# Optimization experiments

Measured on AMD Instinct MI355X. Metric: run time of the kernel, lower is better.

The kernel has to match this reference:

```python
import jax, jax.numpy as jnp
import numpy as np

V, E, H, L = 50257, 1024, 1024, 512


def setup_inputs() -> dict:
    key = jax.random.key(0)
    ks = jax.random.split(key, 12)
    s = 0.02
    return {
        'input': jax.random.randint(ks[0], (1,), 0, V),
        'hidden': jax.random.normal(ks[1], (1, 1, H), dtype=jnp.float32),
        'encoder_outputs': jax.random.normal(ks[2], (L, H), dtype=jnp.float32),
        'emb_table': jax.random.normal(ks[3], (V, E), dtype=jnp.float32) * s,
        'attn_W': jax.random.normal(ks[4], (L, E + H), dtype=jnp.float32) * s,
        'attn_b': jax.random.normal(ks[5], (L,), dtype=jnp.float32) * s,
        'W_ih': jax.random.normal(ks[6], (3 * H, E + H), dtype=jnp.float32) * s,
        'W_hh': jax.random.normal(ks[7], (3 * H, H), dtype=jnp.float32) * s,
        'b_ih': jax.random.normal(ks[8], (3 * H,), dtype=jnp.float32) * s,
        'b_hh': jax.random.normal(ks[9], (3 * H,), dtype=jnp.float32) * s,
        'out_W': jax.random.normal(ks[10], (V, H), dtype=jnp.float32) * s,
        'out_b': jax.random.normal(ks[11], (V,), dtype=jnp.float32) * s,
    }


def reference(input, hidden, encoder_outputs, emb_table, attn_W, attn_b,
              W_ih, W_hh, b_ih, b_hh, out_W, out_b):
    # Dropout is inference-identity here.
    embedded = emb_table[input].reshape(1, E)                      # [1, E]
    h = hidden[0]                                                  # [1, H]
    attn_in = jnp.concatenate([embedded, h], axis=1)               # [1, E+H]
    attn_weights = jax.nn.softmax(attn_in @ attn_W.T + attn_b, axis=1)  # [1, L]
    attn_applied = attn_weights @ encoder_outputs                  # [1, H]
    x = jnp.concatenate([embedded, attn_applied], axis=1)          # [1, E+H]
    # PyTorch GRU cell, gate order (r, z, n)
    gi = x @ W_ih.T + b_ih                                         # [1, 3H]
    gh = h @ W_hh.T + b_hh                                         # [1, 3H]
    i_r, i_z, i_n = gi[:, :H], gi[:, H:2 * H], gi[:, 2 * H:]
    h_r, h_z, h_n = gh[:, :H], gh[:, H:2 * H], gh[:, 2 * H:]
    r = jax.nn.sigmoid(i_r + h_r)
    z = jax.nn.sigmoid(i_z + h_z)
    n = jnp.tanh(i_n + r * h_n)
    h_new = (1.0 - z) * n + z * h                                  # [1, H]
    log_probs = jax.nn.log_softmax(h_new @ out_W.T + out_b, axis=1)  # [1, V]
    return log_probs, h_new[None], attn_weights
```

## Files before the change

### kernel.cpp

```cpp
#include <hip/hip_runtime.h>
#include <math.h>

#define V 50257
#define E 1024
#define H 1024
#define L 512

#define OUT_H  50257
#define OUT_AW 51281

#define WS_S    0
#define WS_X    1024
#define WS_GH   3072
#define WS_GI   6144
#define WS_BM   10240
#define WS_BS   12288

__device__ __forceinline__ float dot4(const float4 a, const float4 b) {
    return a.x * b.x + a.y * b.y + a.z * b.z + a.w * b.w;
}

__device__ __forceinline__ float wave_sum(float v) {
    for (int off = 32; off > 0; off >>= 1) v += __shfl_down(v, off, 64);
    return v;
}

__global__ void k1_scores_gh(const int* __restrict__ input,
                             const float* __restrict__ hidden,
                             const float* __restrict__ emb_table,
                             const float* __restrict__ attn_W,
                             const float* __restrict__ attn_b,
                             const float* __restrict__ W_hh,
                             const float* __restrict__ b_hh,
                             float* __restrict__ ws) {
    const int t = threadIdx.x;
    const int lane = t & 63;
    const int gwave = blockIdx.x * 4 + (t >> 6);
    const float4* h4 = (const float4*)hidden;
    const float* embrow = emb_table + (size_t)input[0] * E;

    if (gwave < L) {
        const float4* emb4 = (const float4*)embrow;
        const float4* w4 = (const float4*)(attn_W + (size_t)gwave * (E + H));
        float acc = 0.f;
#pragma unroll
        for (int k = 0; k < 8; ++k) {
            int i = lane + 64 * k;
            float4 a = (k < 4) ? emb4[i] : h4[i - E / 4];
            acc += dot4(a, w4[i]);
        }
        acc = wave_sum(acc);
        if (lane == 0) ws[WS_S + gwave] = acc + attn_b[gwave];
    } else if (gwave < L + 3 * H) {
        int k = gwave - L;
        const float4* w4 = (const float4*)(W_hh + (size_t)k * H);
        float acc = 0.f;
#pragma unroll
        for (int ii = 0; ii < 4; ++ii) {
            int i = lane + 64 * ii;
            acc += dot4(h4[i], w4[i]);
        }
        acc = wave_sum(acc);
        if (lane == 0) ws[WS_GH + k] = acc + b_hh[k];
    } else if (gwave < 3600) {
        ws[WS_X + E + (gwave - 3584) * 64 + lane] = 0.f;
    } else if (gwave < 3616) {
        int i = (gwave - 3600) * 64 + lane;
        ws[WS_X + i] = embrow[i];
    }
}

__global__ void k2_softmax_applied(const float* __restrict__ enc,
                                   float* __restrict__ ws,
                                   float* __restrict__ out) {
    __shared__ float w[512];
    __shared__ float redm[4], reds[4];
    __shared__ float bmax, bsum;
    const int t = threadIdx.x;
    const int lane = t & 63, wid = t >> 6;

    float v0 = ws[WS_S + t];
    float v1 = ws[WS_S + 256 + t];
    float m = fmaxf(v0, v1);
    for (int off = 32; off > 0; off >>= 1) m = fmaxf(m, __shfl_down(m, off, 64));
    if (lane == 0) redm[wid] = m;
    __syncthreads();
    if (t == 0) bmax = fmaxf(fmaxf(redm[0], redm[1]), fmaxf(redm[2], redm[3]));
    __syncthreads();
    float e0 = expf(v0 - bmax), e1 = expf(v1 - bmax);
    float s = wave_sum(e0 + e1);
    if (lane == 0) reds[wid] = s;
    __syncthreads();
    if (t == 0) bsum = reds[0] + reds[1] + reds[2] + reds[3];
    __syncthreads();
    float inv = 1.f / bsum;
    w[t] = e0 * inv;
    w[256 + t] = e1 * inv;
    if (blockIdx.x == 0) {
        out[OUT_AW + t] = e0 * inv;
        out[OUT_AW + 256 + t] = e1 * inv;
    }
    __syncthreads();

    const int j = (blockIdx.x & 3) * 256 + t;
    const int l0 = (blockIdx.x >> 2) * 64;
    float acc = 0.f;
#pragma unroll 8
    for (int l = l0; l < l0 + 64; ++l)
        acc += w[l] * enc[(size_t)l * H + j];
    atomicAdd(&ws[WS_X + E + j], acc);
}

__global__ void k3_gi(const float* __restrict__ W_ih, const float* __restrict__ b_ih,
                      float* __restrict__ ws) {
    const int lane = threadIdx.x & 63;
    const int gwave = blockIdx.x * 4 + (threadIdx.x >> 6);
    const float4* x4 = (const float4*)(ws + WS_X);
    const float4* w4 = (const float4*)(W_ih + (size_t)gwave * (E + H));
    float acc = 0.f;
#pragma unroll
    for (int k = 0; k < 8; ++k) {
        int i = lane + 64 * k;
        acc += dot4(x4[i], w4[i]);
    }
    acc = wave_sum(acc);
    if (lane == 0) ws[WS_GI + gwave] = acc + b_ih[gwave];
}

__global__ void k4_logits(const float* __restrict__ hidden,
                          const float* __restrict__ out_W,
                          const float* __restrict__ out_b,
                          float* __restrict__ ws,
                          float* __restrict__ out) {
    __shared__ float hn[H];
    __shared__ float wm[4], wsum[4];
    const int t = threadIdx.x;
    const int lane = t & 63, wid = t >> 6;

#pragma unroll
    for (int c = 0; c < 4; ++c) {
        int k = t + 256 * c;
        float gir = ws[WS_GI + k],         ghr = ws[WS_GH + k];
        float giz = ws[WS_GI + H + k],     ghz = ws[WS_GH + H + k];
        float gin = ws[WS_GI + 2 * H + k], ghn = ws[WS_GH + 2 * H + k];
        float r = 1.f / (1.f + expf(-(gir + ghr)));
        float z = 1.f / (1.f + expf(-(giz + ghz)));
        float n = tanhf(gin + r * ghn);
        float v = (1.f - z) * n + z * hidden[k];
        hn[k] = v;
        if (blockIdx.x == 0) out[OUT_H + k] = v;
    }
    __syncthreads();

    const float4* hn4 = (const float4*)hn;
    const int gwave = blockIdx.x * 4 + wid;
    float m = -INFINITY, s = 0.f;
    for (int row = gwave; row < V; row += 8192) {
        const float4* w4 = (const float4*)(out_W + (size_t)row * H);
        float acc = 0.f;
#pragma unroll
        for (int ii = 0; ii < 4; ++ii) {
            int i = lane + 64 * ii;
            acc += dot4(hn4[i], w4[i]);
        }
        acc = wave_sum(acc);
        if (lane == 0) {
            float lg = acc + out_b[row];
            out[row] = lg;
            if (lg > m) { s = s * expf(m - lg) + 1.f; m = lg; }
            else        { s += expf(lg - m); }
        }
    }
    if (lane == 0) { wm[wid] = m; wsum[wid] = s; }
    __syncthreads();
    if (t == 0) {
        float M = fmaxf(fmaxf(wm[0], wm[1]), fmaxf(wm[2], wm[3]));
        float S = wsum[0] * expf(wm[0] - M) + wsum[1] * expf(wm[1] - M)
                + wsum[2] * expf(wm[2] - M) + wsum[3] * expf(wm[3] - M);
        ws[WS_BM + blockIdx.x] = M;
        ws[WS_BS + blockIdx.x] = S;
    }
}

__global__ void k5_logprobs(const float* __restrict__ ws, float* __restrict__ out) {
    __shared__ float redm[4], reds[4];
    __shared__ float off_s;
    const int t = threadIdx.x;
    const int lane = t & 63, wid = t >> 6;
    float m = -INFINITY, s = 0.f;
#pragma unroll
    for (int c = 0; c < 8; ++c) {
        int b = t + 256 * c;
        float bm = ws[WS_BM + b], bs = ws[WS_BS + b];
        float M2 = fmaxf(m, bm);
        s = s * expf(m - M2) + bs * expf(bm - M2);
        m = M2;
    }
    for (int off = 32; off > 0; off >>= 1) {
        float mo = __shfl_down(m, off, 64);
        float so = __shfl_down(s, off, 64);
        float M2 = fmaxf(m, mo);
        s = s * expf(m - M2) + so * expf(mo - M2);
        m = M2;
    }
    if (lane == 0) { redm[wid] = m; reds[wid] = s; }
    __syncthreads();
    if (t == 0) {
        float M = redm[0], S = reds[0];
        for (int i = 1; i < 4; ++i) {
            float M2 = fmaxf(M, redm[i]);
            S = S * expf(M - M2) + reds[i] * expf(redm[i] - M2);
            M = M2;
        }
        off_s = M + logf(S);
    }
    __syncthreads();
    int i = blockIdx.x * 256 + t;
    if (i < V) out[i] -= off_s;
}

extern "C" void kernel_launch(void* const* d_in, const int* in_sizes, int n_in,
                              void* d_out, int out_size, void* d_ws, size_t ws_size,
                              hipStream_t stream) {
    const int*   input   = (const int*)d_in[0];
    const float* hidden  = (const float*)d_in[1];
    const float* enc     = (const float*)d_in[2];
    const float* emb     = (const float*)d_in[3];
    const float* attn_W  = (const float*)d_in[4];
    const float* attn_b  = (const float*)d_in[5];
    const float* W_ih    = (const float*)d_in[6];
    const float* W_hh    = (const float*)d_in[7];
    const float* b_ih    = (const float*)d_in[8];
    const float* b_hh    = (const float*)d_in[9];
    const float* out_W   = (const float*)d_in[10];
    const float* out_b   = (const float*)d_in[11];
    float* out = (float*)d_out;
    float* ws  = (float*)d_ws;

    k1_scores_gh<<<904, 256, 0, stream>>>(input, hidden, emb, attn_W, attn_b, W_hh, b_hh, ws);
    k2_softmax_applied<<<32, 256, 0, stream>>>(enc, ws, out);
    k3_gi<<<768, 256, 0, stream>>>(W_ih, b_ih, ws);
    k4_logits<<<2048, 256, 0, stream>>>(hidden, out_W, out_b, ws, out);
    k5_logprobs<<<197, 256, 0, stream>>>(ws, out);
}
```

Measured before the change: 443.2 us.

## Fuse all stages into one persistent kernel with grid barriers and out_W prefetch

Replaces the five kernel launches with one persistent kernel of 1024 blocks that syncs stages through atomic grid barriers in workspace. While 768 blocks run the attention/GRU-input stages, the other 256 blocks stream out_W rows to warm the cache before the logits stage. The aim is to remove launch gaps and overlap loading the large output matrix with the dependent front stages. It depends on all blocks being co-resident, since the spin barriers would deadlock otherwise (a guard counter bounds the wait), and it adds barrier latency and a memset.

```diff
diff --git a/kernel.cpp b/kernel.cpp
--- a/kernel.cpp
+++ b/kernel.cpp
@@ -14,7 +14,11 @@
 #define WS_GH   3072
 #define WS_GI   6144
 #define WS_BM   10240
-#define WS_BS   12288
+#define WS_BS   11264
+#define WS_BAR  12288
+
+#define NB 1024
+#define NC 768
 
 __device__ __forceinline__ float dot4(const float4 a, const float4 b) {
     return a.x * b.x + a.y * b.y + a.z * b.z + a.w * b.w;
@@ -25,117 +29,153 @@
     return v;
 }
 
-__global__ void k1_scores_gh(const int* __restrict__ input,
-                             const float* __restrict__ hidden,
-                             const float* __restrict__ emb_table,
-                             const float* __restrict__ attn_W,
-                             const float* __restrict__ attn_b,
-                             const float* __restrict__ W_hh,
-                             const float* __restrict__ b_hh,
-                             float* __restrict__ ws) {
+__device__ __forceinline__ void gbar(int* bar, int idx, int target) {
+    __syncthreads();
+    if (threadIdx.x == 0) {
+        __threadfence();
+        __hip_atomic_fetch_add(&bar[idx], 1, __ATOMIC_RELEASE, __HIP_MEMORY_SCOPE_AGENT);
+        int guard = 0;
+        while (__hip_atomic_load(&bar[idx], __ATOMIC_ACQUIRE, __HIP_MEMORY_SCOPE_AGENT) < target) {
+            __builtin_amdgcn_s_sleep(2);
+            if (++guard > (1 << 22)) break;
+        }
+    }
+    __syncthreads();
+    __threadfence();
+}
+
+__global__ __launch_bounds__(256, 4)
+void fused(const int* __restrict__ input,
+           const float* __restrict__ hidden,
+           const float* __restrict__ enc,
+           const float* __restrict__ emb_table,
+           const float* __restrict__ attn_W,
+           const float* __restrict__ attn_b,
+           const float* __restrict__ W_ih,
+           const float* __restrict__ W_hh,
+           const float* __restrict__ b_ih,
+           const float* __restrict__ b_hh,
+           const float* __restrict__ out_W,
+           const float* __restrict__ out_b,
+           float* __restrict__ out,
+           float* __restrict__ ws) {
+    __shared__ float w[512];
+    __shared__ float hn[H];
+    __shared__ float redm[4], reds[4];
+    __shared__ float bmax, bsum, off_s;
+
     const int t = threadIdx.x;
     const int lane = t & 63;
-    const int gwave = blockIdx.x * 4 + (t >> 6);
+    const int wid = t >> 6;
+    const int bid = blockIdx.x;
+    int* bar = (int*)(ws + WS_BAR);
     const float4* h4 = (const float4*)hidden;
-    const float* embrow = emb_table + (size_t)input[0] * E;
-
-    if (gwave < L) {
-        const float4* emb4 = (const float4*)embrow;
-        const float4* w4 = (const float4*)(attn_W + (size_t)gwave * (E + H));
-        float acc = 0.f;
-#pragma unroll
-        for (int k = 0; k < 8; ++k) {
-            int i = lane + 64 * k;
-            float4 a = (k < 4) ? emb4[i] : h4[i - E / 4];
-            acc += dot4(a, w4[i]);
-        }
-        acc = wave_sum(acc);
-        if (lane == 0) ws[WS_S + gwave] = acc + attn_b[gwave];
-    } else if (gwave < L + 3 * H) {
-        int k = gwave - L;
-        const float4* w4 = (const float4*)(W_hh + (size_t)k * H);
-        float acc = 0.f;
-#pragma unroll
-        for (int ii = 0; ii < 4; ++ii) {
-            int i = lane + 64 * ii;
-            acc += dot4(h4[i], w4[i]);
-        }
-        acc = wave_sum(acc);
-        if (lane == 0) ws[WS_GH + k] = acc + b_hh[k];
-    } else if (gwave < 3600) {
-        ws[WS_X + E + (gwave - 3584) * 64 + lane] = 0.f;
-    } else if (gwave < 3616) {
-        int i = (gwave - 3600) * 64 + lane;
-        ws[WS_X + i] = embrow[i];
-    }
-}
-
-__global__ void k2_softmax_applied(const float* __restrict__ enc,
-                                   float* __restrict__ ws,
-                                   float* __restrict__ out) {
-    __shared__ float w[512];
-    __shared__ float redm[4], reds[4];
-    __shared__ float bmax, bsum;
-    const int t = threadIdx.x;
-    const int lane = t & 63, wid = t >> 6;
-
-    float v0 = ws[WS_S + t];
-    float v1 = ws[WS_S + 256 + t];
-    float m = fmaxf(v0, v1);
-    for (int off = 32; off > 0; off >>= 1) m = fmaxf(m, __shfl_down(m, off, 64));
-    if (lane == 0) redm[wid] = m;
-    __syncthreads();
-    if (t == 0) bmax = fmaxf(fmaxf(redm[0], redm[1]), fmaxf(redm[2], redm[3]));
-    __syncthreads();
-    float e0 = expf(v0 - bmax), e1 = expf(v1 - bmax);
-    float s = wave_sum(e0 + e1);
-    if (lane == 0) reds[wid] = s;
-    __syncthreads();
-    if (t == 0) bsum = reds[0] + reds[1] + reds[2] + reds[3];
-    __syncthreads();
-    float inv = 1.f / bsum;
-    w[t] = e0 * inv;
-    w[256 + t] = e1 * inv;
-    if (blockIdx.x == 0) {
-        out[OUT_AW + t] = e0 * inv;
-        out[OUT_AW + 256 + t] = e1 * inv;
-    }
-    __syncthreads();
-
-    const int j = (blockIdx.x & 3) * 256 + t;
-    const int l0 = (blockIdx.x >> 2) * 64;
-    float acc = 0.f;
-#pragma unroll 8
-    for (int l = l0; l < l0 + 64; ++l)
-        acc += w[l] * enc[(size_t)l * H + j];
-    atomicAdd(&ws[WS_X + E + j], acc);
-}
-
-__global__ void k3_gi(const float* __restrict__ W_ih, const float* __restrict__ b_ih,
-                      float* __restrict__ ws) {
-    const int lane = threadIdx.x & 63;
-    const int gwave = blockIdx.x * 4 + (threadIdx.x >> 6);
-    const float4* x4 = (const float4*)(ws + WS_X);
-    const float4* w4 = (const float4*)(W_ih + (size_t)gwave * (E + H));
-    float acc = 0.f;
-#pragma unroll
-    for (int k = 0; k < 8; ++k) {
-        int i = lane + 64 * k;
-        acc += dot4(x4[i], w4[i]);
-    }
-    acc = wave_sum(acc);
-    if (lane == 0) ws[WS_GI + gwave] = acc + b_ih[gwave];
-}
-
-__global__ void k4_logits(const float* __restrict__ hidden,
-                          const float* __restrict__ out_W,
-                          const float* __restrict__ out_b,
-                          float* __restrict__ ws,
-                          float* __restrict__ out) {
-    __shared__ float hn[H];
-    __shared__ float wm[4], wsum[4];
-    const int t = threadIdx.x;
-    const int lane = t & 63, wid = t >> 6;
+
+    if (bid < NC) {
+        const float* embrow = emb_table + (size_t)input[0] * E;
+
+        for (int gw = bid * 4 + wid; gw < 3616; gw += NC * 4) {
+            if (gw < L) {
+                const float4* emb4 = (const float4*)embrow;
+                const float4* w4 = (const float4*)(attn_W + (size_t)gw * (E + H));
+                float acc = 0.f;
+#pragma unroll
+                for (int k = 0; k < 8; ++k) {
+                    int i = lane + 64 * k;
+                    float4 a = (k < 4) ? emb4[i] : h4[i - E / 4];
+                    acc += dot4(a, w4[i]);
+                }
+                acc = wave_sum(acc);
+                if (lane == 0) ws[WS_S + gw] = acc + attn_b[gw];
+            } else if (gw < L + 3 * H) {
+                int k = gw - L;
+                const float4* w4 = (const float4*)(W_hh + (size_t)k * H);
+                float acc = 0.f;
+#pragma unroll
+                for (int ii = 0; ii < 4; ++ii) {
+                    int i = lane + 64 * ii;
+                    acc += dot4(h4[i], w4[i]);
+                }
+                acc = wave_sum(acc);
+                if (lane == 0) ws[WS_GH + k] = acc + b_hh[k];
+            } else if (gw < 3600) {
+                ws[WS_X + E + (gw - 3584) * 64 + lane] = 0.f;
+            } else {
+                int i = (gw - 3600) * 64 + lane;
+                ws[WS_X + i] = embrow[i];
+            }
+        }
+
+        gbar(bar, 0, NC);
+
+        if (bid < 128) {
+            float v0 = ws[WS_S + t];
+            float v1 = ws[WS_S + 256 + t];
+            float m = fmaxf(v0, v1);
+            for (int off = 32; off > 0; off >>= 1) m = fmaxf(m, __shfl_down(m, off, 64));
+            if (lane == 0) redm[wid] = m;
+            __syncthreads();
+            if (t == 0) bmax = fmaxf(fmaxf(redm[0], redm[1]), fmaxf(redm[2], redm[3]));
+            __syncthreads();
+            float e0 = expf(v0 - bmax), e1 = expf(v1 - bmax);
+            float s = wave_sum(e0 + e1);
+            if (lane == 0) reds[wid] = s;
+            __syncthreads();
+            if (t == 0) bsum = reds[0] + reds[1] + reds[2] + reds[3];
+            __syncthreads();
+            float inv = 1.f / bsum;
+            w[t] = e0 * inv;
+            w[256 + t] = e1 * inv;
+            if (bid == 0) {
+                out[OUT_AW + t] = e0 * inv;
+                out[OUT_AW + 256 + t] = e1 * inv;
+            }
+            __syncthreads();
+            const int j = (bid & 3) * 256 + t;
+            const int l0 = (bid >> 2) * 16;
+            float acc = 0.f;
+#pragma unroll
+            for (int l = l0; l < l0 + 16; ++l)
+                acc += w[l] * enc[(size_t)l * H + j];
+            atomicAdd(&ws[WS_X + E + j], acc);
+        }
+
+        gbar(bar, 1, NC);
+
+        {
+            const int gw = bid * 4 + wid;
+            const float4* x4 = (const float4*)(ws + WS_X);
+            const float4* w4 = (const float4*)(W_ih + (size_t)gw * (E + H));
+            float acc = 0.f;
+#pragma unroll
+            for (int k = 0; k < 8; ++k) {
+                int i = lane + 64 * k;
+                acc += dot4(x4[i], w4[i]);
+            }
+            acc = wave_sum(acc);
+            if (lane == 0) ws[WS_GI + gw] = acc + b_ih[gw];
+        }
+
+        gbar(bar, 2, NB);
+    } else {
+        const int pfw = (bid - NC) * 4 + wid;
+        float dummy = 0.f;
+        for (int k = 0; k < 50; ++k) {
+            int row = pfw + k * 1024;
+            if (row >= V) break;
+            const float4* w4 = (const float4*)(out_W + (size_t)row * H);
+#pragma unroll
+            for (int ii = 0; ii < 4; ++ii) {
+                float4 r = w4[lane + 64 * ii];
+                dummy += r.x + r.y + r.z + r.w;
+            }
+            if ((k & 3) == 3 &&
+                __hip_atomic_load(&bar[1], __ATOMIC_RELAXED, __HIP_MEMORY_SCOPE_AGENT) >= NC)
+                break;
+        }
+        asm volatile("" :: "v"(dummy));
+        gbar(bar, 2, NB);
+    }
 
 #pragma unroll
     for (int c = 0; c < 4; ++c) {
@@ -148,75 +188,75 @@
         float n = tanhf(gin + r * ghn);
         float v = (1.f - z) * n + z * hidden[k];
         hn[k] = v;
-        if (blockIdx.x == 0) out[OUT_H + k] = v;
+        if (bid == 0) out[OUT_H + k] = v;
     }
     __syncthreads();
 
-    const float4* hn4 = (const float4*)hn;
-    const int gwave = blockIdx.x * 4 + wid;
-    float m = -INFINITY, s = 0.f;
-    for (int row = gwave; row < V; row += 8192) {
-        const float4* w4 = (const float4*)(out_W + (size_t)row * H);
-        float acc = 0.f;
-#pragma unroll
-        for (int ii = 0; ii < 4; ++ii) {
-            int i = lane + 64 * ii;
-            acc += dot4(hn4[i], w4[i]);
-        }
-        acc = wave_sum(acc);
-        if (lane == 0) {
-            float lg = acc + out_b[row];
-            out[row] = lg;
-            if (lg > m) { s = s * expf(m - lg) + 1.f; m = lg; }
-            else        { s += expf(lg - m); }
-        }
-    }
-    if (lane == 0) { wm[wid] = m; wsum[wid] = s; }
-    __syncthreads();
-    if (t == 0) {
-        float M = fmaxf(fmaxf(wm[0], wm[1]), fmaxf(wm[2], wm[3]));
-        float S = wsum[0] * expf(wm[0] - M) + wsum[1] * expf(wm[1] - M)
-                + wsum[2] * expf(wm[2] - M) + wsum[3] * expf(wm[3] - M);
-        ws[WS_BM + blockIdx.x] = M;
-        ws[WS_BS + blockIdx.x] = S;
-    }
-}
-
-__global__ void k5_logprobs(const float* __restrict__ ws, float* __restrict__ out) {
-    __shared__ float redm[4], reds[4];
-    __shared__ float off_s;
-    const int t = threadIdx.x;
-    const int lane = t & 63, wid = t >> 6;
-    float m = -INFINITY, s = 0.f;
-#pragma unroll
-    for (int c = 0; c < 8; ++c) {
-        int b = t + 256 * c;
-        float bm = ws[WS_BM + b], bs = ws[WS_BS + b];
-        float M2 = fmaxf(m, bm);
-        s = s * expf(m - M2) + bs * expf(bm - M2);
-        m = M2;
-    }
-    for (int off = 32; off > 0; off >>= 1) {
-        float mo = __shfl_down(m, off, 64);
-        float so = __shfl_down(s, off, 64);
-        float M2 = fmaxf(m, mo);
-        s = s * expf(m - M2) + so * expf(mo - M2);
-        m = M2;
-    }
-    if (lane == 0) { redm[wid] = m; reds[wid] = s; }
-    __syncthreads();
-    if (t == 0) {
-        float M = redm[0], S = reds[0];
-        for (int i = 1; i < 4; ++i) {
-            float M2 = fmaxf(M, redm[i]);
-            S = S * expf(M - M2) + reds[i] * expf(redm[i] - M2);
-            M = M2;
-        }
-        off_s = M + logf(S);
-    }
-    __syncthreads();
-    int i = blockIdx.x * 256 + t;
-    if (i < V) out[i] -= off_s;
+    {
+        const float4* hn4 = (const float4*)hn;
+        const int gwave = bid * 4 + wid;
+        float m = -INFINITY, s = 0.f;
+        for (int row = gwave; row < V; row += NB * 4) {
+            const float4* w4 = (const float4*)(out_W + (size_t)row * H);
+            float acc = 0.f;
+#pragma unroll
+            for (int ii = 0; ii < 4; ++ii) {
+                int i = lane + 64 * ii;
+                acc += dot4(hn4[i], w4[i]);
+            }
+            acc = wave_sum(acc);
+            if (lane == 0) {
+                float lg = acc + out_b[row];
+                out[row] = lg;
+                if (lg > m) { s = s * expf(m - lg) + 1.f; m = lg; }
+                else        { s += expf(lg - m); }
+            }
+        }
+        if (lane == 0) { redm[wid] = m; reds[wid] = s; }
+        __syncthreads();
+        if (t == 0) {
+            float M = fmaxf(fmaxf(redm[0], redm[1]), fmaxf(redm[2], redm[3]));
+            float S = reds[0] * expf(redm[0] - M) + reds[1] * expf(redm[1] - M)
+                    + reds[2] * expf(redm[2] - M) + reds[3] * expf(redm[3] - M);
+            ws[WS_BM + bid] = M;
+            ws[WS_BS + bid] = S;
+        }
+    }
+
+    gbar(bar, 3, NB);
+
+    {
+        float m = -INFINITY, s = 0.f;
+#pragma unroll
+        for (int c = 0; c < 4; ++c) {
+            int b = t + 256 * c;
+            float bm = ws[WS_BM + b], bs = ws[WS_BS + b];
+            float M2 = fmaxf(m, bm);
+            s = s * expf(m - M2) + bs * expf(bm - M2);
+            m = M2;
+        }
+        for (int off = 32; off > 0; off >>= 1) {
+            float mo = __shfl_down(m, off, 64);
+            float so = __shfl_down(s, off, 64);
+            float M2 = fmaxf(m, mo);
+            s = s * expf(m - M2) + so * expf(mo - M2);
+            m = M2;
+        }
+        if (lane == 0) { redm[wid] = m; reds[wid] = s; }
+        __syncthreads();
+        if (t == 0) {
+            float M = redm[0], S = reds[0];
+            for (int i = 1; i < 4; ++i) {
+                float M2 = fmaxf(M, redm[i]);
+                S = S * expf(M - M2) + reds[i] * expf(redm[i] - M2);
+                M = M2;
+            }
+            off_s = M + logf(S);
+        }
+        __syncthreads();
+        int i = bid * 256 + t;
+        if (i < V) out[i] -= off_s;
+    }
 }
 
 extern "C" void kernel_launch(void* const* d_in, const int* in_sizes, int n_in,
@@ -237,9 +277,8 @@
     float* out = (float*)d_out;
     float* ws  = (float*)d_ws;
 
-    k1_scores_gh<<<904, 256, 0, stream>>>(input, hidden, emb, attn_W, attn_b, W_hh, b_hh, ws);
-    k2_softmax_applied<<<32, 256, 0, stream>>>(enc, ws, out);
-    k3_gi<<<768, 256, 0, stream>>>(W_ih, b_ih, ws);
-    k4_logits<<<2048, 256, 0, stream>>>(hidden, out_W, out_b, ws, out);
-    k5_logprobs<<<197, 256, 0, stream>>>(ws, out);
-}
+    hipMemsetAsync((char*)d_ws + WS_BAR * sizeof(float), 0, 8 * sizeof(int), stream);
+
+    fused<<<NB, 256, 0, stream>>>(input, hidden, enc, emb, attn_W, attn_b,
+                                  W_ih, W_hh, b_ih, b_hh, out_W, out_b, out, ws);
+}
```

After: 1.229 ms. +177.4%, slower.
